# Performance work log

Hardware: AMD Instinct MI355X
Metric: run time of the kernel (lower is better)

Reference implementation:

```python
import jax, jax.numpy as jnp
import numpy as np

B, C, R, M, N = 8, 16, 16, 512, 512
ASYM = 1e-3


def _rot(a, z):
    # torch: r = (a*z).diff(-1) = a1*z1 - a0*z0 ; i = (a*z[...,[1,0]]).sum(-1) = a0*z1 + a1*z0
    r = a[..., 1] * z[..., 1] - a[..., 0] * z[..., 0]
    i = a[..., 0] * z[..., 1] + a[..., 1] * z[..., 0]
    return jnp.stack([r, i], axis=-1)


def _cmatmul(a, b):
    # complex matmul on trailing [..., P, Q, 2] x [..., Q, S, 2] (equivalent to the A/B einsum trick)
    ar, ai = a[..., 0], a[..., 1]
    br, bi = b[..., 0], b[..., 1]
    return jnp.stack([ar @ br - ai @ bi, ar @ bi + ai @ br], axis=-1)


def setup_inputs() -> dict:
    key = jax.random.key(0)
    ks = jax.random.split(key, 14)
    rn = lambda k, s, sc=1.0: jax.random.normal(k, s, dtype=jnp.float32) * sc
    rot_init = lambda k1, k2: jnp.concatenate(
        [1.0 + rn(k1, (1, C, 1, 1, 1), ASYM), rn(k2, (1, C, 1, 1, 1), ASYM)], axis=-1)
    return {
        "x": rn(ks[0], (B, C)),
        "weights_i": rn(ks[1], (1, 1, M, M, 2), 1.0 / np.log(M * M)),
        "weights_j": rn(ks[2], (1, 1, N, N, 2), 1.0 / np.log(N * N)),
        "weights_base": rn(ks[3], (1, 1, M, N, 2), 1.0 / np.log(M * N)),
        "translate_base": rn(ks[4], (1, C, 1, 1, 2), ASYM),
        "rotate_base": rot_init(ks[5], ks[6]),
        "translate_dynamic": rn(ks[7], (1, C, 1, 1, 2), ASYM),
        "rotate_dynamic": rot_init(ks[8], ks[9]),
        "mod_i": rn(ks[10], (1, C, R, M, 2), 1.0 / np.log(R * M)),
        "mod_j": rn(ks[11], (1, C, R, N, 2)),
        "inversions": -1.0 + rn(ks[12], (1, C, 1, 1, 2), ASYM),
        "mod_transforms": rn(ks[13], (4, C, 2 * C), np.sqrt(2.0 / (3 * C))),
    }


def reference(x, weights_i, weights_j, weights_base, translate_base, rotate_base,
              translate_dynamic, rotate_dynamic, mod_i, mod_j, inversions, mod_transforms):
    Bx = x.shape[0]
    # NOTE: the original computes a rotated/translated `weights` from weights_base,
    # translate_base, rotate_base that is never used afterwards (dead code) -> omitted.
    t = jnp.einsum('bc,kcl->bkl', x, mod_transforms)          # [B,4,2C]
    t = t.reshape(Bx, 4, C, 1, 1, 2)
    # low-rank modulation factors, per component, rotated by dynamic transforms
    mi = _rot(mod_i + t[:, 0], t[:, 1])                        # [B,C,R,M,2]
    mj = _rot(mod_j + t[:, 2], t[:, 3])                        # [B,C,R,N,2]
    # inversion-rotate mod_i then sum over components
    mi = _rot(mi, inversions).sum(axis=1, keepdims=True)       # [B,1,R,M,2]
    # "division-like" inversion for mod_j then sum over components
    denom = (mj * mj).sum(axis=-1, keepdims=True)
    r = (inversions * mj).sum(axis=-1, keepdims=True) / denom
    i = (inversions[..., 0:1] * mj[..., 1:2] - inversions[..., 1:2] * mj[..., 0:1]) / denom
    mj = jnp.concatenate([r, i], axis=-1).sum(axis=1, keepdims=True)  # [B,1,R,N,2]
    # complex outer-product modulation: [B,1,M,R] @ [B,1,R,N] -> [B,1,M,N,2]
    mod = _cmatmul(jnp.swapaxes(mi, -3, -2), mj)
    mr = mod[..., 0]
    mr = (mr - mr.mean(axis=(-2, -1), keepdims=True)) / jnp.std(mr, axis=(-2, -1), ddof=1, keepdims=True)
    mod = jnp.stack([mr, mod[..., 1]], axis=-1)
    # modulate base weights (componentwise, not complex mult)
    wd = weights_base + weights_base * mod                     # [B,1,M,N,2]
    # cross-mixing complex matmuls
    wd = _cmatmul(jnp.swapaxes(wd, -3, -2), weights_i)         # [B,1,N,M,2]
    wd = _cmatmul(jnp.swapaxes(wd, -3, -2), weights_j)         # [B,1,M,N,2]
    # per-component dynamic translate + rotate, sum components, take real part
    wd = wd + translate_dynamic                                # [B,C,M,N,2]
    wd = _rot(wd, rotate_dynamic).sum(axis=1)[..., 0]          # [B,M,N]
    return wd
```

## Files before the change

### kernel.cpp

```cpp
#include <hip/hip_runtime.h>
#include <hip/hip_bf16.h>
#include <math.h>


#define WS_STATS   1296
#define WS_MIS     4096
#define WS_MJS     135168
#define WS_BASET   266240
#define WS_A2      790528
#define WS_B5T     1052672
#define WS_G1X     1314816
#define WS_B2T     3411968
#define WS_GP      7606272
#define WS_CS      7737344

typedef __attribute__((ext_vector_type(8))) short short8;
typedef __attribute__((ext_vector_type(4))) float f32x4;

__device__ __forceinline__ unsigned short f2bf(float f) {
    unsigned int u = __float_as_uint(f);
    u = (u + 0x7FFFu + ((u >> 16) & 1u)) >> 16;
    return (unsigned short)u;
}
__device__ __forceinline__ unsigned int pack2bf(float a, float b) {
    return (unsigned int)f2bf(a) | ((unsigned int)f2bf(b) << 16);
}
__device__ __forceinline__ void load_lds16(const unsigned short* g, unsigned short* l) {
    __builtin_amdgcn_global_load_lds((const __attribute__((address_space(1))) unsigned int*)g,
                                     (__attribute__((address_space(3))) unsigned int*)l, 16, 0, 0);
}

__global__ void k_front(const float* __restrict__ Wi, const float* __restrict__ Wj,
                        const float* __restrict__ base, const float* __restrict__ rd,
                        const float* __restrict__ x, const float* __restrict__ mt,
                        const float* __restrict__ inv, const float* __restrict__ mod_i,
                        const float* __restrict__ mod_j, float* __restrict__ ws) {
    __shared__ __align__(16) char shmem[32 * 33 * 8];
    int blk = blockIdx.x;
    int tid = threadIdx.x;
    if (blk < 768) {
        float2(*tile)[33] = (float2(*)[33])shmem;
        int mode = blk >> 8;
        int idx = blk & 255;
        int bx = idx & 15, by = idx >> 4;
        int tx = tid & 31, ty = tid >> 5;
        const float* src = (mode == 0) ? Wi : (mode == 1) ? Wj : base;
        for (int i = 0; i < 4; i++) {
            int rIn = by * 32 + ty + i * 8;
            int cIn = bx * 32 + tx;
            tile[ty + i * 8][tx] = *(const float2*)(src + ((size_t)rIn * 512 + cIn) * 2);
        }
        __syncthreads();
        if (mode == 0) {
            unsigned int* A2u = (unsigned int*)(ws + WS_A2);
            for (int i = 0; i < 4; i++) {
                int rOut = bx * 32 + ty + i * 8;
                int cOut = by * 32 + tx;
                float2 v = tile[tx][ty + i * 8];
                A2u[(size_t)rOut * 512 + cOut] = pack2bf(v.x, v.y);
            }
        } else if (mode == 1) {
            float ar = 0.f, ai = 0.f;
            for (int c = 0; c < 16; c++) { ar -= rd[2 * c]; ai -= rd[2 * c + 1]; }
            unsigned int* B5u = (unsigned int*)(ws + WS_B5T);
            for (int i = 0; i < 4; i++) {
                int rOut = bx * 32 + ty + i * 8;
                int cOut = by * 32 + tx;
                float2 v = tile[tx][ty + i * 8];
                float wr = ar * v.x - ai * v.y;
                float wi = ar * v.y + ai * v.x;
                B5u[(size_t)rOut * 512 + cOut] = pack2bf(wr, -wi);
            }
        } else {
            float* baseT = ws + WS_BASET;
            for (int i = 0; i < 4; i++) {
                int rOut = bx * 32 + ty + i * 8;
                int cOut = by * 32 + tx;
                *(float2*)(baseT + ((size_t)rOut * 512 + cOut) * 2) = tile[tx][ty + i * 8];
            }
        }
    } else {
        float* tb = (float*)shmem;
        float* deS = (float*)shmem + 128;
        int blk2 = blk - 768;
        bool isMi = blk2 < 256;
        int id = (isMi ? blk2 : blk2 - 256) * 256 + tid;
        int b = id >> 13, rm = id & 8191;
        if (tid < 128) {
            int k = tid >> 5, l = tid & 31;
            float s = 0.f;
            for (int c = 0; c < 16; c++) s += x[b * 16 + c] * mt[(k * 16 + c) * 32 + l];
            tb[tid] = s;
        }
        __syncthreads();
        if (tid < 16) {
            float i0 = inv[2 * tid], i1 = inv[2 * tid + 1];
            float z0 = tb[32 + 2 * tid], z1 = tb[32 + 2 * tid + 1];
            deS[2 * tid]     = i0 * z0 + i1 * z1;
            deS[2 * tid + 1] = i0 * z1 - i1 * z0;
        }
        __syncthreads();
        if (isMi) {
            float acc0 = 0.f, acc1 = 0.f;
            for (int c = 0; c < 16; c++) {
                const float* p = mod_i + (((size_t)c * 8192) + rm) * 2;
                float A0 = p[0] + tb[2 * c], A1 = p[1] + tb[2 * c + 1];
                float d = deS[2 * c], e = deS[2 * c + 1];
                acc0 += d * A0 - e * A1;
                acc1 += e * A0 + d * A1;
            }
            float* dst = ws + WS_MIS + ((size_t)b * 8192 + rm) * 2;
            dst[0] = acc0; dst[1] = acc1;
        } else {
            float acc0 = 0.f, acc1 = 0.f;
            for (int c = 0; c < 16; c++) {
                const float* p = mod_j + (((size_t)c * 8192) + rm) * 2;
                float A0 = p[0] + tb[64 + 2 * c], A1 = p[1] + tb[64 + 2 * c + 1];
                float z0 = tb[96 + 2 * c], z1 = tb[96 + 2 * c + 1];
                float w0 = -z0 * A0 + z1 * A1;
                float w1 =  z1 * A0 + z0 * A1;
                float i0 = inv[2 * c], i1 = inv[2 * c + 1];
                float den = w0 * w0 + w1 * w1;
                acc0 += (i0 * w0 + i1 * w1) / den;
                acc1 += (i0 * w1 - i1 * w0) / den;
            }
            float* dst = ws + WS_MJS + ((size_t)b * 8192 + rm) * 2;
            dst[0] = acc0; dst[1] = acc1;
        }
    }
}

__global__ __launch_bounds__(256) void k_gram1(float* __restrict__ ws) {
    __shared__ float2 Vs[16][66];
    __shared__ float2 Us[16][66];
    int ch = blockIdx.x, b = blockIdx.y, tid = threadIdx.x;
    int r = tid >> 4, r2 = tid & 15;
    const float2* V = (const float2*)(ws + WS_MIS + (size_t)b * 16384);
    const float2* U = (const float2*)(ws + WS_MJS + (size_t)b * 16384);
    int c0 = ch * 64;
    for (int p = 0; p < 4; p++) {
        int f = tid + p * 256;
        int rr = f >> 6, mm = f & 63;
        Vs[rr][mm] = V[rr * 512 + c0 + mm];
        Us[rr][mm] = U[rr * 512 + c0 + mm];
    }
    __syncthreads();
    float Svr = 0, Svi = 0, Tvr = 0, Tvi = 0;
    float Sur = 0, Sui = 0, Tur = 0, Tui = 0;
    float ar = 0, ai = 0, br = 0, bi = 0;
    for (int mm = 0; mm < 64; mm++) {
        float2 v1 = Vs[r][mm], v2 = Vs[r2][mm];
        float2 u1 = Us[r][mm], u2 = Us[r2][mm];
        Svr += v1.x * v2.x - v1.y * v2.y;  Svi += v1.x * v2.y + v1.y * v2.x;
        Tvr += v1.x * v2.x + v1.y * v2.y;  Tvi += v1.y * v2.x - v1.x * v2.y;
        Sur += u1.x * u2.x - u1.y * u2.y;  Sui += u1.x * u2.y + u1.y * u2.x;
        Tur += u1.x * u2.x + u1.y * u2.y;  Tui += u1.y * u2.x - u1.x * u2.y;
        if (r2 == 0) { ar += v1.x; ai += v1.y; br += u1.x; bi += u1.y; }
    }
    float4* g4 = (float4*)(ws + WS_GP + (((size_t)b * 8 + ch) * 256 + tid) * 8);
    g4[0] = make_float4(Svr, Svi, Tvr, Tvi);
    g4[1] = make_float4(Sur, Sui, Tur, Tui);
    if (r2 == 0)
        *(float4*)(ws + WS_CS + (((size_t)b * 8 + ch) * 16 + r) * 4) =
            make_float4(ar, ai, br, bi);
}

__global__ __launch_bounds__(256) void k_bmod(float* __restrict__ ws) {
    const float* mi_s  = ws + WS_MIS;
    const float* mj_s  = ws + WS_MJS;
    const float* baseT = ws + WS_BASET;
    unsigned int* B2T  = (unsigned int*)(ws + WS_B2T);
    int mt = blockIdx.x, nt = blockIdx.y, b = blockIdx.z;
    __shared__ float Ns[16][128];
    __shared__ float Ms[16][128];
    __shared__ float red[256];
    __shared__ float red2[16];
    __shared__ float sStat[2];
    int tid = threadIdx.x, tx = tid & 15, ty = tid >> 4;

    {
        float Svr = 0, Svi = 0, Tvr = 0, Tvi = 0;
        float Sur = 0, Sui = 0, Tur = 0, Tui = 0;
        for (int ch = 0; ch < 8; ch++) {
            const float4* g4 = (const float4*)(ws + WS_GP + (((size_t)b * 8 + ch) * 256 + tid) * 8);
            float4 a0 = g4[0], a1 = g4[1];
            Svr += a0.x; Svi += a0.y; Tvr += a0.z; Tvi += a0.w;
            Sur += a1.x; Sui += a1.y; Tur += a1.z; Tui += a1.w;
        }
        red[tid] = (Sur * Svr - Sui * Svi) + (Tur * Tvr - Tui * Tvi);
        if (tid < 16) {
            float ar = 0, ai = 0, br = 0, bi = 0;
            for (int ch = 0; ch < 8; ch++) {
                float4 c = *(const float4*)(ws + WS_CS + (((size_t)b * 8 + ch) * 16 + tid) * 4);
                ar += c.x; ai += c.y; br += c.z; bi += c.w;
            }
            red2[tid] = br * ar - bi * ai;
        }
        __syncthreads();
        for (int s = 128; s > 0; s >>= 1) {
            if (tid < s) red[tid] += red[tid + s];
            __syncthreads();
        }
        if (tid == 0) {
            float msum = 0.f;
            for (int i = 0; i < 16; i++) msum += red2[i];
            double MN = 262144.0;
            double mu = (double)msum / MN;
            double sumsq = 0.5 * (double)red[0];
            double var = (sumsq - MN * mu * mu) / (MN - 1.0);
            if (var < 1e-30) var = 1e-30;
            sStat[0] = (float)mu;
            sStat[1] = (float)(1.0 / sqrt(var));
        }
    }

    const float* Nb = mj_s + (size_t)b * 16384;
    const float* Mb = mi_s + (size_t)b * 16384;
    int n0 = nt * 64, m0 = mt * 64;
    for (int i = 0; i < 4; i++) {
        int flat = tid + i * 256;
        int col = flat & 63, r = flat >> 6;
        float2 sa = *(const float2*)(Nb + ((size_t)r * 512 + n0 + col) * 2);
        Ns[r][col * 2] = sa.x; Ns[r][col * 2 + 1] = sa.y;
        float2 sb = *(const float2*)(Mb + ((size_t)r * 512 + m0 + col) * 2);
        Ms[r][col * 2] = sb.x; Ms[r][col * 2 + 1] = sb.y;
    }
    __syncthreads();
    float cr[4][4] = {}, ci[4][4] = {};
    for (int r = 0; r < 16; r++) {
        float nr[4], ni[4], mr[4], mi_[4];
        for (int i = 0; i < 4; i++) { nr[i] = Ns[r][(ty * 4 + i) * 2]; ni[i] = Ns[r][(ty * 4 + i) * 2 + 1]; }
        for (int j = 0; j < 4; j++) { mr[j] = Ms[r][(tx + j * 16) * 2]; mi_[j] = Ms[r][(tx + j * 16) * 2 + 1]; }
        for (int i = 0; i < 4; i++)
            for (int j = 0; j < 4; j++) {
                cr[i][j] += nr[i] * mr[j] - ni[i] * mi_[j];
                ci[i][j] += nr[i] * mi_[j] + ni[i] * mr[j];
            }
    }
    float mu = sStat[0], rstd = sStat[1];
    unsigned int* Bb = B2T + (size_t)b * 524288;
    for (int i = 0; i < 4; i++) {
        int n = n0 + ty * 4 + i;
        for (int j = 0; j < 4; j++) {
            int m = m0 + tx + j * 16;
            float2 bs = *(const float2*)(baseT + ((size_t)n * 512 + m) * 2);
            float wr = bs.x * (1.f + (cr[i][j] - mu) * rstd);
            float wi = bs.y * (1.f + ci[i][j]);
            Bb[(size_t)(2 * n) * 512 + m]     = pack2bf(wr, -wi);
            Bb[(size_t)(2 * n + 1) * 512 + m] = pack2bf(wi, wr);
        }
    }
}

template <int TM, int TN, bool OUT_BF16>
__global__ __launch_bounds__(256) void k_gemm(const unsigned short* __restrict__ Aall,
                                              const unsigned short* __restrict__ BTall,
                                              void* __restrict__ Call,
                                              const float* __restrict__ td,
                                              const float* __restrict__ rd,
                                              size_t a_bs, size_t bt_bs, size_t c_bs,
                                              int ngl) {
    constexpr int K = 1024;
    constexpr int NK = K / 64;
    constexpr int IT = TM / 32, JT = TN / 32;
    constexpr int STG = (TM + TN) * 64;
    constexpr int SMC = OUT_BF16 ? TM * (TN + 8) : 0;
    constexpr int SMEMN = (2 * STG > SMC) ? 2 * STG : SMC;
    __shared__ __align__(16) unsigned short smem[SMEMN];

    const int tid = threadIdx.x;
    const int b = blockIdx.z;
    const unsigned short* A  = Aall  + (size_t)b * a_bs;
    const unsigned short* BT = BTall + (size_t)b * bt_bs;
    const int mBase = blockIdx.y * TM;
    const int nBase = blockIdx.x * TN;
    const int wave = tid >> 6, lane = tid & 63;
    const int wm = wave >> 1, wn = wave & 1;
    const int l15 = lane & 15, q = lane >> 4;

    f32x4 acc[IT][JT];
    for (int i = 0; i < IT; i++)
        for (int j = 0; j < JT; j++) acc[i][j] = (f32x4)0.f;

    auto stage = [&](int k0, int buf) {
        unsigned short* As = smem + buf * STG;
        unsigned short* Bs = As + TM * 64;
#pragma unroll
        for (int p = 0; p < TM / 32; p++) {
            int flat = tid + p * 256;
            int r = flat >> 3, c = flat & 7;
            int gc = (c ^ (r & 7)) << 3;
            load_lds16(A + (size_t)(mBase + r) * K + k0 + gc, &As[flat << 3]);
        }
#pragma unroll
        for (int p = 0; p < TN / 32; p++) {
            int flat = tid + p * 256;
            int r = flat >> 3, c = flat & 7;
            int gc = (c ^ (r & 7)) << 3;
            load_lds16(BT + (size_t)(nBase + r) * K + k0 + gc, &Bs[flat << 3]);
        }
    };

    stage(0, 0);
    for (int kt = 0; kt < NK; kt++) {
        __syncthreads();
        if (kt + 1 < NK) stage((kt + 1) * 64, (kt + 1) & 1);
        const unsigned short* As = smem + (kt & 1) * STG;
        const unsigned short* Bs = As + TM * 64;
#pragma unroll
        for (int ks = 0; ks < 2; ks++) {
            short8 af[IT], bfr[JT];
#pragma unroll
            for (int t = 0; t < IT; t++) {
                int ra = wm * (TM / 2) + t * 16 + l15;
                int ja = (ks * 4 + q) ^ (ra & 7);
                af[t] = *(const short8*)&As[ra * 64 + ja * 8];
            }
#pragma unroll
            for (int t = 0; t < JT; t++) {
                int rb = wn * (TN / 2) + t * 16 + l15;
                int jb = (ks * 4 + q) ^ (rb & 7);
                bfr[t] = *(const short8*)&Bs[rb * 64 + jb * 8];
            }
#pragma unroll
            for (int i = 0; i < IT; i++)
#pragma unroll
                for (int j = 0; j < JT; j++)
                    acc[i][j] = __builtin_amdgcn_mfma_f32_16x16x32_bf16(af[i], bfr[j], acc[i][j], 0, 0, 0);
        }
    }

    if constexpr (OUT_BF16) {
        __syncthreads();
        unsigned short* Cs = smem;
#pragma unroll
        for (int i = 0; i < IT; i++) {
            int row0 = wm * (TM / 2) + i * 16 + q * 4;
#pragma unroll
            for (int j = 0; j < JT; j++) {
                int col = wn * (TN / 2) + j * 16 + l15;
#pragma unroll
                for (int r = 0; r < 4; r++)
                    Cs[(row0 + r) * (TN + 8) + col] = f2bf(acc[i][j][r]);
            }
        }
        __syncthreads();
        unsigned short* C = (unsigned short*)Call + (size_t)b * c_bs;
#pragma unroll
        for (int p = 0; p < TM * TN / 2048; p++) {
            int flat = tid + p * 256;
            int r = flat / (TN / 8), c = flat % (TN / 8);
            short8 v = *(const short8*)&Cs[r * (TN + 8) + c * 8];
            *(short8*)(C + (size_t)(mBase + r) * ngl + nBase + c * 8) = v;
        }
    } else {
        float CC = 0.f;
        for (int c = 0; c < 16; c++) CC += td[2 * c + 1] * rd[2 * c + 1] - td[2 * c] * rd[2 * c];
        float* C = (float*)Call + (size_t)b * c_bs;
#pragma unroll
        for (int i = 0; i < IT; i++) {
            int row0 = mBase + wm * (TM / 2) + i * 16 + q * 4;
#pragma unroll
            for (int j = 0; j < JT; j++) {
                int col = nBase + wn * (TN / 2) + j * 16 + l15;
#pragma unroll
                for (int r = 0; r < 4; r++)
                    C[(size_t)(row0 + r) * ngl + col] = acc[i][j][r] + CC;
            }
        }
    }
}

extern "C" void kernel_launch(void* const* d_in, const int* in_sizes, int n_in,
                              void* d_out, int out_size, void* d_ws, size_t ws_size,
                              hipStream_t stream) {
    const float* x    = (const float*)d_in[0];
    const float* Wi   = (const float*)d_in[1];
    const float* Wj   = (const float*)d_in[2];
    const float* base = (const float*)d_in[3];
    const float* td   = (const float*)d_in[6];
    const float* rd   = (const float*)d_in[7];
    const float* modi = (const float*)d_in[8];
    const float* modj = (const float*)d_in[9];
    const float* inv  = (const float*)d_in[10];
    const float* mt   = (const float*)d_in[11];
    float* ws  = (float*)d_ws;
    float* out = (float*)d_out;

    unsigned short* A2  = (unsigned short*)(ws + WS_A2);
    unsigned short* B5T = (unsigned short*)(ws + WS_B5T);
    unsigned short* B2T = (unsigned short*)(ws + WS_B2T);
    unsigned short* G1X = (unsigned short*)(ws + WS_G1X);

    k_front<<<1280, 256, 0, stream>>>(Wi, Wj, base, rd, x, mt, inv, modi, modj, ws);
    k_gram1<<<dim3(8, 8), 256, 0, stream>>>(ws);
    k_bmod<<<dim3(8, 8, 8), 256, 0, stream>>>(ws);
    k_gemm<128, 64, true><<<dim3(16, 4, 8), 256, 0, stream>>>(
        A2, B2T, (void*)G1X, td, rd, (size_t)0, (size_t)1048576, (size_t)524288, 1024);
    k_gemm<64, 128, false><<<dim3(4, 8, 8), 256, 0, stream>>>(
        G1X, B5T, (void*)out, td, rd, (size_t)524288, (size_t)0, (size_t)262144, 512);
}
```

Before: 131.2 us.

## Fuse Gram partial-sum computation into front kernel, removing separate gram kernel

```diff
diff --git a/kernel.cpp b/kernel.cpp
--- a/kernel.cpp
+++ b/kernel.cpp
@@ -3,7 +3,6 @@
 #include <math.h>
 
 
-#define WS_STATS   1296
 #define WS_MIS     4096
 #define WS_MJS     135168
 #define WS_BASET   266240
@@ -11,8 +10,10 @@
 #define WS_B5T     1052672
 #define WS_G1X     1314816
 #define WS_B2T     3411968
-#define WS_GP      7606272
-#define WS_CS      7737344
+#define WS_GPV     7606272
+#define WS_GPU     7737344
+#define WS_CSV     7868416
+#define WS_CSU     7872512
 
 typedef __attribute__((ext_vector_type(8))) short short8;
 typedef __attribute__((ext_vector_type(4))) float f32x4;
@@ -35,7 +36,7 @@
                         const float* __restrict__ x, const float* __restrict__ mt,
                         const float* __restrict__ inv, const float* __restrict__ mod_i,
                         const float* __restrict__ mod_j, float* __restrict__ ws) {
-    __shared__ __align__(16) char shmem[32 * 33 * 8];
+    __shared__ __align__(16) char shmem[8448];
     int blk = blockIdx.x;
     int tid = threadIdx.x;
     if (blk < 768) {
@@ -79,32 +80,41 @@
                 *(float2*)(baseT + ((size_t)rOut * 512 + cOut) * 2) = tile[tx][ty + i * 8];
             }
         }
-    } else {
-        float* tb = (float*)shmem;
-        float* deS = (float*)shmem + 128;
-        int blk2 = blk - 768;
-        bool isMi = blk2 < 256;
-        int id = (isMi ? blk2 : blk2 - 256) * 256 + tid;
-        int b = id >> 13, rm = id & 8191;
-        if (tid < 128) {
-            int k = tid >> 5, l = tid & 31;
-            float s = 0.f;
-            for (int c = 0; c < 16; c++) s += x[b * 16 + c] * mt[(k * 16 + c) * 32 + l];
-            tb[tid] = s;
-        }
-        __syncthreads();
-        if (tid < 16) {
-            float i0 = inv[2 * tid], i1 = inv[2 * tid + 1];
-            float z0 = tb[32 + 2 * tid], z1 = tb[32 + 2 * tid + 1];
-            deS[2 * tid]     = i0 * z0 + i1 * z1;
-            deS[2 * tid + 1] = i0 * z1 - i1 * z0;
-        }
-        __syncthreads();
+        return;
+    }
+
+    float* tb  = (float*)shmem;
+    float* deS = (float*)shmem + 128;
+    float2(*Vs)[33] = (float2(*)[33])((float*)shmem + 160);
+    int blk2 = blk - 768;
+    bool isMi = blk2 < 128;
+    int idx = isMi ? blk2 : blk2 - 128;
+    int b = idx >> 4, ch = idx & 15;
+    int m0 = ch * 32;
+    if (tid < 128) {
+        int k = tid >> 5, l = tid & 31;
+        float s = 0.f;
+        for (int c = 0; c < 16; c++) s += x[b * 16 + c] * mt[(k * 16 + c) * 32 + l];
+        tb[tid] = s;
+    }
+    __syncthreads();
+    if (tid < 16) {
+        float i0 = inv[2 * tid], i1 = inv[2 * tid + 1];
+        float z0 = tb[32 + 2 * tid], z1 = tb[32 + 2 * tid + 1];
+        deS[2 * tid]     = i0 * z0 + i1 * z1;
+        deS[2 * tid + 1] = i0 * z1 - i1 * z0;
+    }
+    __syncthreads();
+    for (int pp = 0; pp < 2; pp++) {
+        int p = tid + pp * 256;
+        int r = p >> 5, ml = p & 31;
+        int rm = r * 512 + m0 + ml;
+        float acc0, acc1;
         if (isMi) {
-            float acc0 = 0.f, acc1 = 0.f;
+            acc0 = 0.f; acc1 = 0.f;
             for (int c = 0; c < 16; c++) {
-                const float* p = mod_i + (((size_t)c * 8192) + rm) * 2;
-                float A0 = p[0] + tb[2 * c], A1 = p[1] + tb[2 * c + 1];
+                const float* pg = mod_i + (((size_t)c * 8192) + rm) * 2;
+                float A0 = pg[0] + tb[2 * c], A1 = pg[1] + tb[2 * c + 1];
                 float d = deS[2 * c], e = deS[2 * c + 1];
                 acc0 += d * A0 - e * A1;
                 acc1 += e * A0 + d * A1;
@@ -112,10 +122,10 @@
             float* dst = ws + WS_MIS + ((size_t)b * 8192 + rm) * 2;
             dst[0] = acc0; dst[1] = acc1;
         } else {
-            float acc0 = 0.f, acc1 = 0.f;
+            acc0 = 0.f; acc1 = 0.f;
             for (int c = 0; c < 16; c++) {
-                const float* p = mod_j + (((size_t)c * 8192) + rm) * 2;
-                float A0 = p[0] + tb[64 + 2 * c], A1 = p[1] + tb[64 + 2 * c + 1];
+                const float* pg = mod_j + (((size_t)c * 8192) + rm) * 2;
+                float A0 = pg[0] + tb[64 + 2 * c], A1 = pg[1] + tb[64 + 2 * c + 1];
                 float z0 = tb[96 + 2 * c], z1 = tb[96 + 2 * c + 1];
                 float w0 = -z0 * A0 + z1 * A1;
                 float w1 =  z1 * A0 + z0 * A1;
@@ -127,42 +137,26 @@
             float* dst = ws + WS_MJS + ((size_t)b * 8192 + rm) * 2;
             dst[0] = acc0; dst[1] = acc1;
         }
-    }
-}
-
-__global__ __launch_bounds__(256) void k_gram1(float* __restrict__ ws) {
-    __shared__ float2 Vs[16][66];
-    __shared__ float2 Us[16][66];
-    int ch = blockIdx.x, b = blockIdx.y, tid = threadIdx.x;
-    int r = tid >> 4, r2 = tid & 15;
-    const float2* V = (const float2*)(ws + WS_MIS + (size_t)b * 16384);
-    const float2* U = (const float2*)(ws + WS_MJS + (size_t)b * 16384);
-    int c0 = ch * 64;
-    for (int p = 0; p < 4; p++) {
-        int f = tid + p * 256;
-        int rr = f >> 6, mm = f & 63;
-        Vs[rr][mm] = V[rr * 512 + c0 + mm];
-        Us[rr][mm] = U[rr * 512 + c0 + mm];
+        Vs[r][ml] = make_float2(acc0, acc1);
     }
     __syncthreads();
-    float Svr = 0, Svi = 0, Tvr = 0, Tvi = 0;
-    float Sur = 0, Sui = 0, Tur = 0, Tui = 0;
-    float ar = 0, ai = 0, br = 0, bi = 0;
-    for (int mm = 0; mm < 64; mm++) {
-        float2 v1 = Vs[r][mm], v2 = Vs[r2][mm];
-        float2 u1 = Us[r][mm], u2 = Us[r2][mm];
-        Svr += v1.x * v2.x - v1.y * v2.y;  Svi += v1.x * v2.y + v1.y * v2.x;
-        Tvr += v1.x * v2.x + v1.y * v2.y;  Tvi += v1.y * v2.x - v1.x * v2.y;
-        Sur += u1.x * u2.x - u1.y * u2.y;  Sui += u1.x * u2.y + u1.y * u2.x;
-        Tur += u1.x * u2.x + u1.y * u2.y;  Tui += u1.y * u2.x - u1.x * u2.y;
-        if (r2 == 0) { ar += v1.x; ai += v1.y; br += u1.x; bi += u1.y; }
-    }
-    float4* g4 = (float4*)(ws + WS_GP + (((size_t)b * 8 + ch) * 256 + tid) * 8);
-    g4[0] = make_float4(Svr, Svi, Tvr, Tvi);
-    g4[1] = make_float4(Sur, Sui, Tur, Tui);
-    if (r2 == 0)
-        *(float4*)(ws + WS_CS + (((size_t)b * 8 + ch) * 16 + r) * 4) =
-            make_float4(ar, ai, br, bi);
+    {
+        int r = tid >> 4, r2 = tid & 15;
+        float Sr = 0, Si = 0, Tr = 0, Ti = 0;
+        float ar = 0, ai = 0;
+        for (int mm = 0; mm < 32; mm++) {
+            float2 v1 = Vs[r][mm], v2 = Vs[r2][mm];
+            Sr += v1.x * v2.x - v1.y * v2.y;  Si += v1.x * v2.y + v1.y * v2.x;
+            Tr += v1.x * v2.x + v1.y * v2.y;  Ti += v1.y * v2.x - v1.x * v2.y;
+            if (r2 == 0) { ar += v1.x; ai += v1.y; }
+        }
+        float* gp = ws + (isMi ? WS_GPV : WS_GPU);
+        *(float4*)(gp + (((size_t)b * 256 + tid) * 16 + ch) * 4) = make_float4(Sr, Si, Tr, Ti);
+        if (r2 == 0) {
+            float* cs = ws + (isMi ? WS_CSV : WS_CSU);
+            *(float2*)(cs + (((size_t)b * 16 + ch) * 16 + r) * 2) = make_float2(ar, ai);
+        }
+    }
 }
 
 __global__ __launch_bounds__(256) void k_bmod(float* __restrict__ ws) {
@@ -181,18 +175,20 @@
     {
         float Svr = 0, Svi = 0, Tvr = 0, Tvi = 0;
         float Sur = 0, Sui = 0, Tur = 0, Tui = 0;
-        for (int ch = 0; ch < 8; ch++) {
-            const float4* g4 = (const float4*)(ws + WS_GP + (((size_t)b * 8 + ch) * 256 + tid) * 8);
-            float4 a0 = g4[0], a1 = g4[1];
+        const float4* gv = (const float4*)(ws + WS_GPV + ((size_t)b * 256 + tid) * 64);
+        const float4* gu = (const float4*)(ws + WS_GPU + ((size_t)b * 256 + tid) * 64);
+        for (int ch = 0; ch < 16; ch++) {
+            float4 a0 = gv[ch], a1 = gu[ch];
             Svr += a0.x; Svi += a0.y; Tvr += a0.z; Tvi += a0.w;
             Sur += a1.x; Sui += a1.y; Tur += a1.z; Tui += a1.w;
         }
         red[tid] = (Sur * Svr - Sui * Svi) + (Tur * Tvr - Tui * Tvi);
         if (tid < 16) {
             float ar = 0, ai = 0, br = 0, bi = 0;
-            for (int ch = 0; ch < 8; ch++) {
-                float4 c = *(const float4*)(ws + WS_CS + (((size_t)b * 8 + ch) * 16 + tid) * 4);
-                ar += c.x; ai += c.y; br += c.z; bi += c.w;
+            for (int ch = 0; ch < 16; ch++) {
+                float2 cv = *(const float2*)(ws + WS_CSV + (((size_t)b * 16 + ch) * 16 + tid) * 2);
+                float2 cu = *(const float2*)(ws + WS_CSU + (((size_t)b * 16 + ch) * 16 + tid) * 2);
+                ar += cv.x; ai += cv.y; br += cu.x; bi += cu.y;
             }
             red2[tid] = br * ar - bi * ai;
         }
@@ -392,8 +388,7 @@
     unsigned short* B2T = (unsigned short*)(ws + WS_B2T);
     unsigned short* G1X = (unsigned short*)(ws + WS_G1X);
 
-    k_front<<<1280, 256, 0, stream>>>(Wi, Wj, base, rd, x, mt, inv, modi, modj, ws);
-    k_gram1<<<dim3(8, 8), 256, 0, stream>>>(ws);
+    k_front<<<1024, 256, 0, stream>>>(Wi, Wj, base, rd, x, mt, inv, modi, modj, ws);
     k_bmod<<<dim3(8, 8, 8), 256, 0, stream>>>(ws);
     k_gemm<128, 64, true><<<dim3(16, 4, 8), 256, 0, stream>>>(
         A2, B2T, (void*)G1X, td, rd, (size_t)0, (size_t)1048576, (size_t)524288, 1024);
```

Result: slower. 157.6 us (+20.1%).
